# Optimization experiments

Hardware: AMD Instinct MI355X
Metric: run time of the kernel (lower is better)

Reference implementation:

```python
import jax, jax.numpy as jnp
import numpy as np

B, S, D = 1, 2048, 4096
H, KVH, HD = 32, 8, 128
ROPE_THETA = 10000.0


def setup_inputs() -> dict:
    key = jax.random.key(0)
    k1, k2, k3, k4, k5 = jax.random.split(key, 5)
    scale = D ** -0.5
    return {
        "hidden_states": jax.random.normal(k1, (B, S, D), dtype=jnp.float32),
        "position_ids": jnp.arange(S, dtype=jnp.int64).reshape(1, S),
        "Wq": jax.random.normal(k2, (H * HD, D), dtype=jnp.float32) * scale,
        "Wk": jax.random.normal(k3, (KVH * HD, D), dtype=jnp.float32) * scale,
        "Wv": jax.random.normal(k4, (KVH * HD, D), dtype=jnp.float32) * scale,
        "Wo": jax.random.normal(k5, (D, H * HD), dtype=jnp.float32) * scale,
    }


def _rotate_half(x):
    x1, x2 = x[..., : HD // 2], x[..., HD // 2 :]
    return jnp.concatenate((-x2, x1), axis=-1)


def reference(hidden_states, position_ids, Wq, Wk, Wv, Wo):
    b, s, d = hidden_states.shape
    # projections: nn.Linear applies x @ W.T
    q = jnp.einsum("bsd,ed->bse", hidden_states, Wq).reshape(b, s, H, HD).transpose(0, 2, 1, 3)
    k = jnp.einsum("bsd,ed->bse", hidden_states, Wk).reshape(b, s, KVH, HD).transpose(0, 2, 1, 3)
    v = jnp.einsum("bsd,ed->bse", hidden_states, Wv).reshape(b, s, KVH, HD).transpose(0, 2, 1, 3)
    # rotary embedding (default rope: inv_freq = theta^(-2i/d), attention_scaling = 1)
    inv_freq = 1.0 / (ROPE_THETA ** (jnp.arange(0, HD, 2, dtype=jnp.float32) / HD))
    pos = position_ids.astype(jnp.float32)  # [Bp, S]
    freqs = pos[:, :, None] * inv_freq[None, None, :]  # [Bp, S, HD/2]
    emb = jnp.concatenate((freqs, freqs), axis=-1)  # [Bp, S, HD]
    cos = jnp.cos(emb)[:, None, :, :]  # unsqueeze head dim
    sin = jnp.sin(emb)[:, None, :, :]
    q = q * cos + _rotate_half(q) * sin
    k = k * cos + _rotate_half(k) * sin
    # GQA: expand kv heads to match query heads
    groups = H // KVH
    k = jnp.repeat(k, groups, axis=1)
    v = jnp.repeat(v, groups, axis=1)
    # causal attention, scaling = head_dim^-0.5
    scores = jnp.einsum("bhqd,bhkd->bhqk", q, k) * (HD ** -0.5)
    causal = jnp.tril(jnp.ones((s, s), dtype=bool))
    scores = jnp.where(causal[None, None], scores, jnp.finfo(scores.dtype).min)
    attn = jax.nn.softmax(scores, axis=-1)
    out = jnp.einsum("bhqk,bhkd->bhqd", attn, v)
    out = out.transpose(0, 2, 1, 3).reshape(b, s, H * HD)
    return jnp.einsum("bse,de->bsd", out, Wo)
```

## Files before the change

### kernel.cpp

```cpp
#include <hip/hip_runtime.h>
#include <stdint.h>

typedef unsigned short u16;
typedef __attribute__((ext_vector_type(4))) float f32x4;
typedef __attribute__((ext_vector_type(8))) short bf16x8;

static constexpr int S   = 2048;
static constexpr int DM  = 4096;
static constexpr int NH  = 32;
static constexpr int NKV = 8;
static constexpr int HD  = 128;
static constexpr int LDQ = 5120;

__device__ __forceinline__ u16 f2bf(float f) {
    union { float f; unsigned u; } v; v.f = f;
    return (u16)((v.u + 0x7FFFu + ((v.u >> 16) & 1u)) >> 16);
}
__device__ __forceinline__ float bf2f(u16 h) {
    union { unsigned u; float f; } v; v.u = ((unsigned)h) << 16;
    return v.f;
}
__device__ __forceinline__ unsigned pk2bf(float lo, float hi) {
    unsigned r;
    asm("v_cvt_pk_bf16_f32 %0, %1, %2" : "=v"(r) : "v"(lo), "v"(hi));
    return r;
}

__device__ __forceinline__ void mfma16(f32x4& d, bf16x8 a, bf16x8 b) {
    asm("v_mfma_f32_16x16x32_bf16 %0, %1, %2, %0" : "+v"(d) : "v"(a), "v"(b));
}

__device__ __forceinline__ void gload_lds16(const u16* g, u16* lds) {
    __builtin_amdgcn_global_load_lds((__attribute__((address_space(1))) void*)g,
                                     (__attribute__((address_space(3))) void*)lds,
                                     16, 0, 0);
}

__global__ __launch_bounds__(256) void cvt_all(const float* __restrict__ X,
                                               const float* __restrict__ Wq,
                                               const float* __restrict__ Wk,
                                               const float* __restrict__ Wv,
                                               const float* __restrict__ Wo,
                                               u16* __restrict__ out) {
    const int n4 = 12582912;
    int i = blockIdx.x * blockDim.x + threadIdx.x;
    int stride = gridDim.x * blockDim.x;
    for (; i < n4; i += stride) {
        float4 v;
        if (i < 2097152)       v = ((const float4*)X)[i];
        else if (i < 6291456)  v = ((const float4*)Wq)[i - 2097152];
        else if (i < 7340032)  v = ((const float4*)Wk)[i - 6291456];
        else if (i < 8388608)  v = ((const float4*)Wv)[i - 7340032];
        else                   v = ((const float4*)Wo)[i - 8388608];
        ushort4 o;
        o.x = f2bf(v.x); o.y = f2bf(v.y); o.z = f2bf(v.z); o.w = f2bf(v.w);
        ((ushort4*)out)[i] = o;
    }
}

__global__ __launch_bounds__(256) void rope_table_kernel(float2* __restrict__ tbl) {
    int i = blockIdx.x * blockDim.x + threadIdx.x;
    if (i >= S * 64) return;
    int p = i >> 6, j = i & 63;
    float inv = powf(10000.0f, -(float)j / 64.0f);
    float a = (float)p * inv;
    tbl[i] = make_float2(cosf(a), sinf(a));
}

__global__ __launch_bounds__(256) void rope2_kernel(u16* __restrict__ X,
                                                    const float2* __restrict__ tbl,
                                                    float qscale) {
    int i = blockIdx.x * blockDim.x + threadIdx.x;
    const int total = S * 40 * 64;
    if (i >= total) return;
    int dd = i & 63;
    int t2 = i >> 6;
    int hh = t2 % 40;
    int s  = t2 / 40;
    size_t base;
    float scale;
    if (hh < 32) { base = (size_t)s * LDQ + hh * HD + dd;               scale = qscale; }
    else         { base = (size_t)s * LDQ + 4096 + (hh - 32) * HD + dd; scale = 1.0f;   }
    float x1 = bf2f(X[base]);
    float x2 = bf2f(X[base + 64]);
    float2 cs = tbl[(s << 6) + dd];
    X[base]      = f2bf((x1 * cs.x - x2 * cs.y) * scale);
    X[base + 64] = f2bf((x2 * cs.x + x1 * cs.y) * scale);
}

__global__ __launch_bounds__(256)
void gemm_bt(const u16* __restrict__ A, const u16* __restrict__ Bt,
             float* __restrict__ C, int M, int N, int K, int lda, int ldb, int ldc) {
    __shared__ u16 Al[128 * 64];
    __shared__ u16 Bl[128 * 64];
    const int t = threadIdx.x;
    const int w = t >> 6, l = t & 63;
    const int r16 = l & 15, g4 = l >> 4;
    const int m0 = blockIdx.y * 128, n0 = blockIdx.x * 128;
    const int wr = (w >> 1) * 64, wc = (w & 1) * 64;

    f32x4 acc[4][4];
#pragma unroll
    for (int i = 0; i < 4; ++i)
#pragma unroll
        for (int j = 0; j < 4; ++j) acc[i][j] = f32x4{0.f, 0.f, 0.f, 0.f};

    for (int kt = 0; kt < K; kt += 64) {
#pragma unroll
        for (int i = 0; i < 4; ++i) {
            int c = i * 256 + t;
            int r = c >> 3, s = (c & 7) ^ (r & 7);
            gload_lds16(A + (size_t)(m0 + r) * lda + kt + (s << 3),
                        Al + ((i * 256 + w * 64) << 3));
        }
#pragma unroll
        for (int i = 0; i < 4; ++i) {
            int c = i * 256 + t;
            int r = c >> 3, s = (c & 7) ^ (r & 7);
            gload_lds16(Bt + (size_t)(n0 + r) * ldb + kt + (s << 3),
                        Bl + ((i * 256 + w * 64) << 3));
        }
        asm volatile("s_waitcnt vmcnt(0)" ::: "memory");
        __syncthreads();

#pragma unroll
        for (int kk = 0; kk < 2; ++kk) {
            bf16x8 af[4], bfr[4];
#pragma unroll
            for (int mi = 0; mi < 4; ++mi) {
                int r = wr + mi * 16 + r16;
                af[mi] = *(const bf16x8*)((const char*)Al +
                          ((r * 128 + kk * 64 + g4 * 16) ^ ((r & 7) << 4)));
            }
#pragma unroll
            for (int ni = 0; ni < 4; ++ni) {
                int r = wc + ni * 16 + r16;
                bfr[ni] = *(const bf16x8*)((const char*)Bl +
                           ((r * 128 + kk * 64 + g4 * 16) ^ ((r & 7) << 4)));
            }
#pragma unroll
            for (int mi = 0; mi < 4; ++mi)
#pragma unroll
                for (int ni = 0; ni < 4; ++ni)
                    mfma16(acc[mi][ni], af[mi], bfr[ni]);
        }
        __syncthreads();
    }

    const int rb = g4 * 4;
#pragma unroll
    for (int mi = 0; mi < 4; ++mi)
#pragma unroll
        for (int ni = 0; ni < 4; ++ni) {
            const int n = n0 + wc + ni * 16 + r16;
            const int mbase = m0 + wr + mi * 16 + rb;
#pragma unroll
            for (int j = 0; j < 4; ++j)
                C[(size_t)(mbase + j) * ldc + n] = acc[mi][ni][j];
        }
}

__global__ __launch_bounds__(256)
void gemm_qkv(const u16* __restrict__ A, const u16* __restrict__ Bt,
              u16* __restrict__ Cqk, u16* __restrict__ Vt) {
    __shared__ u16 Al[128 * 64];
    __shared__ u16 Bl[128 * 64];
    const int t = threadIdx.x;
    const int w = t >> 6, l = t & 63;
    const int r16 = l & 15, g4 = l >> 4;
    const int m0 = blockIdx.y * 128, n0 = blockIdx.x * 128;
    const int wr = (w >> 1) * 64, wc = (w & 1) * 64;

    f32x4 acc[4][4];
#pragma unroll
    for (int i = 0; i < 4; ++i)
#pragma unroll
        for (int j = 0; j < 4; ++j) acc[i][j] = f32x4{0.f, 0.f, 0.f, 0.f};

    for (int kt = 0; kt < DM; kt += 64) {
#pragma unroll
        for (int i = 0; i < 4; ++i) {
            int c = i * 256 + t;
            int r = c >> 3, s = (c & 7) ^ (r & 7);
            gload_lds16(A + (size_t)(m0 + r) * DM + kt + (s << 3),
                        Al + ((i * 256 + w * 64) << 3));
        }
#pragma unroll
        for (int i = 0; i < 4; ++i) {
            int c = i * 256 + t;
            int r = c >> 3, s = (c & 7) ^ (r & 7);
            gload_lds16(Bt + (size_t)(n0 + r) * DM + kt + (s << 3),
                        Bl + ((i * 256 + w * 64) << 3));
        }
        asm volatile("s_waitcnt vmcnt(0)" ::: "memory");
        __syncthreads();

#pragma unroll
        for (int kk = 0; kk < 2; ++kk) {
            bf16x8 af[4], bfr[4];
#pragma unroll
            for (int mi = 0; mi < 4; ++mi) {
                int r = wr + mi * 16 + r16;
                af[mi] = *(const bf16x8*)((const char*)Al +
                          ((r * 128 + kk * 64 + g4 * 16) ^ ((r & 7) << 4)));
            }
#pragma unroll
            for (int ni = 0; ni < 4; ++ni) {
                int r = wc + ni * 16 + r16;
                bfr[ni] = *(const bf16x8*)((const char*)Bl +
                           ((r * 128 + kk * 64 + g4 * 16) ^ ((r & 7) << 4)));
            }
#pragma unroll
            for (int mi = 0; mi < 4; ++mi)
#pragma unroll
                for (int ni = 0; ni < 4; ++ni)
                    mfma16(acc[mi][ni], af[mi], bfr[ni]);
        }
        __syncthreads();
    }

    const int rb = g4 * 4;
    if (n0 < 5120) {
#pragma unroll
        for (int mi = 0; mi < 4; ++mi)
#pragma unroll
            for (int ni = 0; ni < 4; ++ni) {
                const int n = n0 + wc + ni * 16 + r16;
                const int mbase = m0 + wr + mi * 16 + rb;
#pragma unroll
                for (int j = 0; j < 4; ++j)
                    Cqk[(size_t)(mbase + j) * LDQ + n] = f2bf(acc[mi][ni][j]);
            }
    } else {
#pragma unroll
        for (int mi = 0; mi < 4; ++mi)
#pragma unroll
            for (int ni = 0; ni < 4; ++ni) {
                const int n = n0 + wc + ni * 16 + r16 - 5120;
                const int mbase = m0 + wr + mi * 16 + rb;
                ushort4 v4;
                v4.x = f2bf(acc[mi][ni][0]); v4.y = f2bf(acc[mi][ni][1]);
                v4.z = f2bf(acc[mi][ni][2]); v4.w = f2bf(acc[mi][ni][3]);
                *(ushort4*)&Vt[(size_t)n * S + mbase] = v4;
            }
    }
}

__global__ __launch_bounds__(256, 3)
void attn_fwd(const u16* __restrict__ QK, const u16* __restrict__ Vt,
              u16* __restrict__ O) {
    __shared__ u16 Kl[2][64 * 128];
    __shared__ u16 Vl[2][128 * 64];
    __shared__ u16 Pl[4 * 16 * 64];

    const int t = threadIdx.x;
    const int w = t >> 6, l = t & 63;
    const int r16 = l & 15, g4 = l >> 4;
    const int h = blockIdx.y;
    const int kvh = h >> 2;
    const int p = blockIdx.x;
    const int q0A = p * 64, q0B = (31 - p) * 64;
    const int ntA = p + 1, ntB = 32 - p;

    const u16* Kg = QK + 4096 + kvh * HD;
    const u16* Vg = Vt + (size_t)(kvh * HD) * S;
    u16* Pb = &Pl[w * 1024];

    bf16x8 qfA[4], qfB[4];
    {
        const u16* Qg = QK + h * HD;
        const size_t qrA = (size_t)(q0A + w * 16 + r16) * LDQ;
        const size_t qrB = (size_t)(q0B + w * 16 + r16) * LDQ;
#pragma unroll
        for (int kg = 0; kg < 4; ++kg) {
            qfA[kg] = *(const bf16x8*)&Qg[qrA + kg * 32 + g4 * 8];
            qfB[kg] = *(const bf16x8*)&Qg[qrB + kg * 32 + g4 * 8];
        }
    }

    f32x4 accA[8], accB[8];
    float mA[4], lA[4], mB[4], lB[4];
#pragma unroll
    for (int i = 0; i < 8; ++i) { accA[i] = f32x4{0,0,0,0}; accB[i] = f32x4{0,0,0,0}; }
#pragma unroll
    for (int j = 0; j < 4; ++j) { mA[j] = -3.0e38f; lA[j] = 0.f; mB[j] = -3.0e38f; lB[j] = 0.f; }

    auto stage = [&](int tk, int b) {
        const int kv0 = tk * 64;
#pragma unroll
        for (int i = 0; i < 4; ++i) {
            int c = i * 256 + t;
            int r = c >> 4, s = (c & 15) ^ (r & 7);
            gload_lds16(Kg + (size_t)(kv0 + r) * LDQ + (s << 3),
                        &Kl[b][0] + ((i * 256 + w * 64) << 3));
        }
#pragma unroll
        for (int i = 0; i < 4; ++i) {
            int c = i * 256 + t;
            int r = c >> 3, s = (c & 7) ^ (r & 7);
            gload_lds16(Vg + (size_t)r * S + kv0 + (s << 3),
                        &Vl[b][0] + ((i * 256 + w * 64) << 3));
        }
    };

    auto compute = [&](f32x4 (&acco)[8], float (&mrun)[4], float (&lrun)[4],
                       const bf16x8 (&qf)[4], int q0, int tk, bool maskit, int b) {
        const int kv0 = tk * 64;
        const u16* Kb = &Kl[b][0];
        const u16* Vb = &Vl[b][0];

        f32x4 sc[4];
#pragma unroll
        for (int ni = 0; ni < 4; ++ni) sc[ni] = f32x4{0,0,0,0};
        __builtin_amdgcn_s_setprio(1);
#pragma unroll
        for (int kg = 0; kg < 4; ++kg) {
#pragma unroll
            for (int ni = 0; ni < 4; ++ni) {
                int row = ni * 16 + r16;
                int bb = (row * 256 + kg * 64 + g4 * 16) ^ ((row & 7) << 4);
                bf16x8 kf = *(const bf16x8*)((const char*)Kb + bb);
                mfma16(sc[ni], qf[kg], kf);
            }
        }
        __builtin_amdgcn_s_setprio(0);

        float vmax[4];
        bool grow = false;
#pragma unroll
        for (int j = 0; j < 4; ++j) {
            if (maskit) {
                const int qg = q0 + w * 16 + g4 * 4 + j;
#pragma unroll
                for (int ni = 0; ni < 4; ++ni)
                    if (kv0 + ni * 16 + r16 > qg) sc[ni][j] = -3.0e38f;
            }
            float v = fmaxf(fmaxf(sc[0][j], sc[1][j]), fmaxf(sc[2][j], sc[3][j]));
            v = fmaxf(v, __shfl_xor(v, 1, 16));
            v = fmaxf(v, __shfl_xor(v, 2, 16));
            v = fmaxf(v, __shfl_xor(v, 4, 16));
            v = fmaxf(v, __shfl_xor(v, 8, 16));
            vmax[j] = v;
            grow = grow || (v > mrun[j] + 11.5f);
        }
        float fac[4] = {1.f, 1.f, 1.f, 1.f};
        if (__any(grow)) {
#pragma unroll
            for (int j = 0; j < 4; ++j) {
                float nm = fmaxf(mrun[j], vmax[j]);
                fac[j] = exp2f(mrun[j] - nm);
                mrun[j] = nm;
            }
#pragma unroll
            for (int i = 0; i < 8; ++i)
#pragma unroll
                for (int j = 0; j < 4; ++j) acco[i][j] *= fac[j];
        }
#pragma unroll
        for (int j = 0; j < 4; ++j) {
            float p0 = exp2f(sc[0][j] - mrun[j]);
            float p1 = exp2f(sc[1][j] - mrun[j]);
            float p2 = exp2f(sc[2][j] - mrun[j]);
            float p3 = exp2f(sc[3][j] - mrun[j]);
            sc[0][j] = p0; sc[1][j] = p1; sc[2][j] = p2; sc[3][j] = p3;
            float s2 = (p0 + p1) + (p2 + p3);
            s2 += __shfl_xor(s2, 1, 16);
            s2 += __shfl_xor(s2, 2, 16);
            s2 += __shfl_xor(s2, 4, 16);
            s2 += __shfl_xor(s2, 8, 16);
            lrun[j] = lrun[j] * fac[j] + s2;
        }

        {
            char* pp = (char*)Pb;
            const int rb_ = g4 * 4;
#pragma unroll
            for (int ni = 0; ni < 4; ++ni) {
                unsigned r01 = pk2bf(sc[ni][0], sc[ni][1]);
                unsigned r23 = pk2bf(sc[ni][2], sc[ni][3]);
                const int col2 = (ni * 16 + r16) << 1;
                *(u16*)(pp + (((rb_ + 0) * 128 + col2) ^ (((rb_ + 0) & 7) << 4))) = (u16)r01;
                *(u16*)(pp + (((rb_ + 1) * 128 + col2) ^ (((rb_ + 1) & 7) << 4))) = (u16)(r01 >> 16);
                *(u16*)(pp + (((rb_ + 2) * 128 + col2) ^ (((rb_ + 2) & 7) << 4))) = (u16)r23;
                *(u16*)(pp + (((rb_ + 3) * 128 + col2) ^ (((rb_ + 3) & 7) << 4))) = (u16)(r23 >> 16);
            }
        }
        asm volatile("s_waitcnt lgkmcnt(0)" ::: "memory");
        __builtin_amdgcn_sched_barrier(0);

        int pb0 = (r16 * 128 + g4 * 16) ^ ((r16 & 7) << 4);
        bf16x8 pf0 = *(const bf16x8*)((const char*)Pb + pb0);
        bf16x8 pf1 = *(const bf16x8*)((const char*)Pb + (pb0 ^ 64));
        __builtin_amdgcn_s_setprio(1);
#pragma unroll
        for (int ni = 0; ni < 8; ++ni) {
            int row = ni * 16 + r16;
            int bb = (row * 128 + g4 * 16) ^ ((row & 7) << 4);
            bf16x8 v0 = *(const bf16x8*)((const char*)Vb + bb);
            mfma16(acco[ni], pf0, v0);
            bf16x8 v1 = *(const bf16x8*)((const char*)Vb + (bb ^ 64));
            mfma16(acco[ni], pf1, v1);
        }
        __builtin_amdgcn_s_setprio(0);
    };

    auto epilogue = [&](f32x4 (&acco)[8], float (&lrun)[4], int q0) {
        float rl[4];
#pragma unroll
        for (int j = 0; j < 4; ++j) rl[j] = 1.0f / lrun[j];
#pragma unroll
        for (int ni = 0; ni < 8; ++ni)
#pragma unroll
            for (int j = 0; j < 4; ++j) {
                const int qg = q0 + w * 16 + g4 * 4 + j;
                O[(size_t)qg * DM + h * HD + ni * 16 + r16] = f2bf(acco[ni][j] * rl[j]);
            }
    };

    stage(0, 0);
    asm volatile("s_waitcnt vmcnt(0)" ::: "memory");
    __syncthreads();
    int buf = 0;

    for (int tk = 0; tk < ntB; ++tk) {
        if (tk + 1 < ntB) stage(tk + 1, buf ^ 1);
        compute(accB, mB, lB, qfB, q0B, tk, tk == ntB - 1, buf);
        if (tk < ntA) compute(accA, mA, lA, qfA, q0A, tk, tk == ntA - 1, buf);
        asm volatile("s_waitcnt vmcnt(0)" ::: "memory");
        __syncthreads();
        buf ^= 1;
    }
    epilogue(accA, lA, q0A);
    epilogue(accB, lB, q0B);
}

extern "C" void kernel_launch(void* const* d_in, const int* in_sizes, int n_in,
                              void* d_out, int out_size, void* d_ws, size_t ws_size,
                              hipStream_t stream) {
    const float* X  = (const float*)d_in[0];
    const float* Wq = (const float*)d_in[2];
    const float* Wk = (const float*)d_in[3];
    const float* Wv = (const float*)d_in[4];
    const float* Wo = (const float*)d_in[5];

    char* ws = (char*)d_ws;
    u16*    Xbf  = (u16*)(ws + 0);
    u16*    Wqkv = (u16*)(ws + 16777216);
    u16*    Wobf = (u16*)(ws + 67108864);
    u16*    QKb  = (u16*)(ws + 100663296);
    u16*    Vtbf = (u16*)(ws + 121634816);
    u16*    Obf  = (u16*)(ws + 125829120);
    float2* tbl  = (float2*)(ws + 142606336);
    if (ws_size < 143654912ull) return;

    dim3 blk(256);

    cvt_all<<<2048, blk, 0, stream>>>(X, Wq, Wk, Wv, Wo, (u16*)ws);
    rope_table_kernel<<<(S * 64 + 255) / 256, blk, 0, stream>>>(tbl);

    gemm_qkv<<<dim3(48, 16), blk, 0, stream>>>(Xbf, Wqkv, QKb, Vtbf);

    rope2_kernel<<<(S * 40 * 64 + 255) / 256, blk, 0, stream>>>(
        QKb, tbl, 0.08838834764831845f * 1.4426950408889634f);

    attn_fwd<<<dim3(16, NH), blk, 0, stream>>>(QKb, Vtbf, Obf);

    gemm_bt<<<dim3(DM / 128, S / 128), blk, 0, stream>>>(
        Obf, Wobf, (float*)d_out, S, DM, DM, DM, DM, DM);
}
```

Baseline: 362.5 us.

## Process two query heads sharing a KV head per attention block

The attention kernel now has each block handle one 64-row query tile for two adjacent heads that share a KV head. Previously each block paired two causal query tiles of a single head. Each K fragment loaded from LDS now feeds MFMAs for both heads, and each staged K/V tile is reused twice, cutting LDS reads and global K/V traffic per unit of work. Causal load balance now comes from interleaving short and long tiles through the block index rather than pairing them inside a block, so block runtimes vary more. Launch bounds drop to 2 waves-per-EU to make room for the doubled register state.

```diff
diff --git a/kernel.cpp b/kernel.cpp
--- a/kernel.cpp
+++ b/kernel.cpp
@@ -246,44 +246,45 @@
     }
 }
 
-__global__ __launch_bounds__(256, 3)
+__global__ __launch_bounds__(256, 2)
 void attn_fwd(const u16* __restrict__ QK, const u16* __restrict__ Vt,
               u16* __restrict__ O) {
     __shared__ u16 Kl[2][64 * 128];
     __shared__ u16 Vl[2][128 * 64];
-    __shared__ u16 Pl[4 * 16 * 64];
+    __shared__ u16 Pl[4 * 1024];
 
     const int t = threadIdx.x;
     const int w = t >> 6, l = t & 63;
     const int r16 = l & 15, g4 = l >> 4;
-    const int h = blockIdx.y;
-    const int kvh = h >> 2;
-    const int p = blockIdx.x;
-    const int q0A = p * 64, q0B = (31 - p) * 64;
-    const int ntA = p + 1, ntB = 32 - p;
+    const int xx = blockIdx.x;
+    const int tq = (xx & 1) ? (31 - (xx >> 1)) : (xx >> 1);
+    const int hp = blockIdx.y;
+    const int h0 = hp << 1;
+    const int kvh = hp >> 1;
+    const int q0 = tq * 64;
+    const int nt = tq + 1;
 
     const u16* Kg = QK + 4096 + kvh * HD;
     const u16* Vg = Vt + (size_t)(kvh * HD) * S;
     u16* Pb = &Pl[w * 1024];
 
-    bf16x8 qfA[4], qfB[4];
+    bf16x8 qf0[4], qf1[4];
     {
-        const u16* Qg = QK + h * HD;
-        const size_t qrA = (size_t)(q0A + w * 16 + r16) * LDQ;
-        const size_t qrB = (size_t)(q0B + w * 16 + r16) * LDQ;
+        const u16* Qg = QK + h0 * HD;
+        const size_t qr = (size_t)(q0 + w * 16 + r16) * LDQ;
 #pragma unroll
         for (int kg = 0; kg < 4; ++kg) {
-            qfA[kg] = *(const bf16x8*)&Qg[qrA + kg * 32 + g4 * 8];
-            qfB[kg] = *(const bf16x8*)&Qg[qrB + kg * 32 + g4 * 8];
-        }
-    }
-
-    f32x4 accA[8], accB[8];
-    float mA[4], lA[4], mB[4], lB[4];
-#pragma unroll
-    for (int i = 0; i < 8; ++i) { accA[i] = f32x4{0,0,0,0}; accB[i] = f32x4{0,0,0,0}; }
-#pragma unroll
-    for (int j = 0; j < 4; ++j) { mA[j] = -3.0e38f; lA[j] = 0.f; mB[j] = -3.0e38f; lB[j] = 0.f; }
+            qf0[kg] = *(const bf16x8*)&Qg[qr + kg * 32 + g4 * 8];
+            qf1[kg] = *(const bf16x8*)&Qg[qr + HD + kg * 32 + g4 * 8];
+        }
+    }
+
+    f32x4 acc0[8], acc1[8];
+    float mr0[4], lr0[4], mr1[4], lr1[4];
+#pragma unroll
+    for (int i = 0; i < 8; ++i) { acc0[i] = f32x4{0,0,0,0}; acc1[i] = f32x4{0,0,0,0}; }
+#pragma unroll
+    for (int j = 0; j < 4; ++j) { mr0[j] = -3.0e38f; lr0[j] = 0.f; mr1[j] = -3.0e38f; lr1[j] = 0.f; }
 
     auto stage = [&](int tk, int b) {
         const int kv0 = tk * 64;
@@ -303,28 +304,8 @@
         }
     };
 
-    auto compute = [&](f32x4 (&acco)[8], float (&mrun)[4], float (&lrun)[4],
-                       const bf16x8 (&qf)[4], int q0, int tk, bool maskit, int b) {
-        const int kv0 = tk * 64;
-        const u16* Kb = &Kl[b][0];
-        const u16* Vb = &Vl[b][0];
-
-        f32x4 sc[4];
-#pragma unroll
-        for (int ni = 0; ni < 4; ++ni) sc[ni] = f32x4{0,0,0,0};
-        __builtin_amdgcn_s_setprio(1);
-#pragma unroll
-        for (int kg = 0; kg < 4; ++kg) {
-#pragma unroll
-            for (int ni = 0; ni < 4; ++ni) {
-                int row = ni * 16 + r16;
-                int bb = (row * 256 + kg * 64 + g4 * 16) ^ ((row & 7) << 4);
-                bf16x8 kf = *(const bf16x8*)((const char*)Kb + bb);
-                mfma16(sc[ni], qf[kg], kf);
-            }
-        }
-        __builtin_amdgcn_s_setprio(0);
-
+    auto soft_pv = [&](f32x4 (&sc)[4], float (&mrun)[4], float (&lrun)[4],
+                       f32x4 (&acco)[8], const u16* Vb, int kv0, bool maskit) {
         float vmax[4];
         bool grow = false;
 #pragma unroll
@@ -404,34 +385,58 @@
         __builtin_amdgcn_s_setprio(0);
     };
 
-    auto epilogue = [&](f32x4 (&acco)[8], float (&lrun)[4], int q0) {
-        float rl[4];
-#pragma unroll
-        for (int j = 0; j < 4; ++j) rl[j] = 1.0f / lrun[j];
-#pragma unroll
-        for (int ni = 0; ni < 8; ++ni)
-#pragma unroll
-            for (int j = 0; j < 4; ++j) {
-                const int qg = q0 + w * 16 + g4 * 4 + j;
-                O[(size_t)qg * DM + h * HD + ni * 16 + r16] = f2bf(acco[ni][j] * rl[j]);
-            }
-    };
-
     stage(0, 0);
     asm volatile("s_waitcnt vmcnt(0)" ::: "memory");
     __syncthreads();
     int buf = 0;
 
-    for (int tk = 0; tk < ntB; ++tk) {
-        if (tk + 1 < ntB) stage(tk + 1, buf ^ 1);
-        compute(accB, mB, lB, qfB, q0B, tk, tk == ntB - 1, buf);
-        if (tk < ntA) compute(accA, mA, lA, qfA, q0A, tk, tk == ntA - 1, buf);
+    for (int tk = 0; tk < nt; ++tk) {
+        if (tk + 1 < nt) stage(tk + 1, buf ^ 1);
+        const int kv0 = tk * 64;
+        const bool maskit = (tk == nt - 1);
+        const u16* Kb = &Kl[buf][0];
+        const u16* Vb = &Vl[buf][0];
+
+        f32x4 sc0[4], sc1[4];
+#pragma unroll
+        for (int ni = 0; ni < 4; ++ni) { sc0[ni] = f32x4{0,0,0,0}; sc1[ni] = f32x4{0,0,0,0}; }
+        __builtin_amdgcn_s_setprio(1);
+#pragma unroll
+        for (int kg = 0; kg < 4; ++kg) {
+#pragma unroll
+            for (int ni = 0; ni < 4; ++ni) {
+                int row = ni * 16 + r16;
+                int bb = (row * 256 + kg * 64 + g4 * 16) ^ ((row & 7) << 4);
+                bf16x8 kf = *(const bf16x8*)((const char*)Kb + bb);
+                mfma16(sc0[ni], qf0[kg], kf);
+                mfma16(sc1[ni], qf1[kg], kf);
+            }
+        }
+        __builtin_amdgcn_s_setprio(0);
+
+        soft_pv(sc0, mr0, lr0, acc0, Vb, kv0, maskit);
+        __builtin_amdgcn_sched_barrier(0);
+        soft_pv(sc1, mr1, lr1, acc1, Vb, kv0, maskit);
+
         asm volatile("s_waitcnt vmcnt(0)" ::: "memory");
         __syncthreads();
         buf ^= 1;
     }
-    epilogue(accA, lA, q0A);
-    epilogue(accB, lB, q0B);
+
+    {
+        float rl0[4], rl1[4];
+#pragma unroll
+        for (int j = 0; j < 4; ++j) { rl0[j] = 1.0f / lr0[j]; rl1[j] = 1.0f / lr1[j]; }
+#pragma unroll
+        for (int ni = 0; ni < 8; ++ni)
+#pragma unroll
+            for (int j = 0; j < 4; ++j) {
+                const int qg = q0 + w * 16 + g4 * 4 + j;
+                const int dd = ni * 16 + r16;
+                O[(size_t)qg * DM + h0 * HD + dd]      = f2bf(acc0[ni][j] * rl0[j]);
+                O[(size_t)qg * DM + h0 * HD + HD + dd] = f2bf(acc1[ni][j] * rl1[j]);
+            }
+    }
 }
 
 extern "C" void kernel_launch(void* const* d_in, const int* in_sizes, int n_in,
@@ -463,7 +468,7 @@
     rope2_kernel<<<(S * 40 * 64 + 255) / 256, blk, 0, stream>>>(
         QKb, tbl, 0.08838834764831845f * 1.4426950408889634f);
 
-    attn_fwd<<<dim3(16, NH), blk, 0, stream>>>(QKb, Vtbf, Obf);
+    attn_fwd<<<dim3(32, 16), blk, 0, stream>>>(QKb, Vtbf, Obf);
 
     gemm_bt<<<dim3(DM / 128, S / 128), blk, 0, stream>>>(
         Obf, Wobf, (float*)d_out, S, DM, DM, DM, DM, DM);
```

Result: slower. 416.0 us (+14.8%).

## Transpose QK^T MFMA so each lane owns one query row for softmax

Applied to the files above, without the earlier changes.

Swaps the MFMA operand order for the score computation so each lane holds 16 scores of a single query row instead of 4 rows. The row max and sum then reduce mostly in registers, with two cross-lane shuffles instead of four per row, and each row keeps a single running max and sum. P is written to LDS as packed 32-bit stores rather than 16-bit scatter stores. Rescale factors and reciprocals are broadcast back to the accumulator layout with shuffles. The launch bounds occupancy hint also drops from 3 to 2, which gives the compiler more registers at the cost of fewer resident waves.

```diff
diff --git a/kernel.cpp b/kernel.cpp
--- a/kernel.cpp
+++ b/kernel.cpp
@@ -246,12 +246,12 @@
     }
 }
 
-__global__ __launch_bounds__(256, 3)
+__global__ __launch_bounds__(256, 2)
 void attn_fwd(const u16* __restrict__ QK, const u16* __restrict__ Vt,
               u16* __restrict__ O) {
     __shared__ u16 Kl[2][64 * 128];
     __shared__ u16 Vl[2][128 * 64];
-    __shared__ u16 Pl[4 * 16 * 64];
+    __shared__ u16 Pl[4 * 1024];
 
     const int t = threadIdx.x;
     const int w = t >> 6, l = t & 63;
@@ -279,11 +279,9 @@
     }
 
     f32x4 accA[8], accB[8];
-    float mA[4], lA[4], mB[4], lB[4];
+    float mA = -3.0e38f, lA = 0.f, mB = -3.0e38f, lB = 0.f;
 #pragma unroll
     for (int i = 0; i < 8; ++i) { accA[i] = f32x4{0,0,0,0}; accB[i] = f32x4{0,0,0,0}; }
-#pragma unroll
-    for (int j = 0; j < 4; ++j) { mA[j] = -3.0e38f; lA[j] = 0.f; mB[j] = -3.0e38f; lB[j] = 0.f; }
 
     auto stage = [&](int tk, int b) {
         const int kv0 = tk * 64;
@@ -303,7 +301,7 @@
         }
     };
 
-    auto compute = [&](f32x4 (&acco)[8], float (&mrun)[4], float (&lrun)[4],
+    auto compute = [&](f32x4 (&acco)[8], float& mrun, float& lrun,
                        const bf16x8 (&qf)[4], int q0, int tk, bool maskit, int b) {
         const int kv0 = tk * 64;
         const u16* Kb = &Kl[b][0];
@@ -320,69 +318,64 @@
                 int row = ni * 16 + r16;
                 int bb = (row * 256 + kg * 64 + g4 * 16) ^ ((row & 7) << 4);
                 bf16x8 kf = *(const bf16x8*)((const char*)Kb + bb);
-                mfma16(sc[ni], qf[kg], kf);
+                mfma16(sc[ni], kf, qf[kg]);
             }
         }
         __builtin_amdgcn_s_setprio(0);
 
-        float vmax[4];
-        bool grow = false;
-#pragma unroll
-        for (int j = 0; j < 4; ++j) {
-            if (maskit) {
-                const int qg = q0 + w * 16 + g4 * 4 + j;
-#pragma unroll
-                for (int ni = 0; ni < 4; ++ni)
-                    if (kv0 + ni * 16 + r16 > qg) sc[ni][j] = -3.0e38f;
-            }
-            float v = fmaxf(fmaxf(sc[0][j], sc[1][j]), fmaxf(sc[2][j], sc[3][j]));
-            v = fmaxf(v, __shfl_xor(v, 1, 16));
-            v = fmaxf(v, __shfl_xor(v, 2, 16));
-            v = fmaxf(v, __shfl_xor(v, 4, 16));
-            v = fmaxf(v, __shfl_xor(v, 8, 16));
-            vmax[j] = v;
-            grow = grow || (v > mrun[j] + 11.5f);
-        }
-        float fac[4] = {1.f, 1.f, 1.f, 1.f};
-        if (__any(grow)) {
-#pragma unroll
-            for (int j = 0; j < 4; ++j) {
-                float nm = fmaxf(mrun[j], vmax[j]);
-                fac[j] = exp2f(mrun[j] - nm);
-                mrun[j] = nm;
-            }
+        const int qg = q0 + (w << 4) + r16;
+        if (maskit) {
+#pragma unroll
+            for (int ni = 0; ni < 4; ++ni)
+#pragma unroll
+                for (int j = 0; j < 4; ++j)
+                    if (kv0 + ni * 16 + g4 * 4 + j > qg) sc[ni][j] = -3.0e38f;
+        }
+
+        float v = fmaxf(fmaxf(fmaxf(sc[0][0], sc[0][1]), fmaxf(sc[0][2], sc[0][3])),
+                        fmaxf(fmaxf(sc[1][0], sc[1][1]), fmaxf(sc[1][2], sc[1][3])));
+        v = fmaxf(v, fmaxf(fmaxf(fmaxf(sc[2][0], sc[2][1]), fmaxf(sc[2][2], sc[2][3])),
+                           fmaxf(fmaxf(sc[3][0], sc[3][1]), fmaxf(sc[3][2], sc[3][3]))));
+        v = fmaxf(v, __shfl_xor(v, 16));
+        v = fmaxf(v, __shfl_xor(v, 32));
+
+        float facl = 1.f;
+        if (__any(v > mrun + 11.5f)) {
+            float nm = fmaxf(mrun, v);
+            facl = exp2f(mrun - nm);
+            mrun = nm;
+            float fj[4];
+#pragma unroll
+            for (int j = 0; j < 4; ++j) fj[j] = __shfl(facl, g4 * 4 + j, 16);
 #pragma unroll
             for (int i = 0; i < 8; ++i)
 #pragma unroll
-                for (int j = 0; j < 4; ++j) acco[i][j] *= fac[j];
-        }
-#pragma unroll
-        for (int j = 0; j < 4; ++j) {
-            float p0 = exp2f(sc[0][j] - mrun[j]);
-            float p1 = exp2f(sc[1][j] - mrun[j]);
-            float p2 = exp2f(sc[2][j] - mrun[j]);
-            float p3 = exp2f(sc[3][j] - mrun[j]);
-            sc[0][j] = p0; sc[1][j] = p1; sc[2][j] = p2; sc[3][j] = p3;
-            float s2 = (p0 + p1) + (p2 + p3);
-            s2 += __shfl_xor(s2, 1, 16);
-            s2 += __shfl_xor(s2, 2, 16);
-            s2 += __shfl_xor(s2, 4, 16);
-            s2 += __shfl_xor(s2, 8, 16);
-            lrun[j] = lrun[j] * fac[j] + s2;
-        }
+                for (int j = 0; j < 4; ++j) acco[i][j] *= fj[j];
+        }
+#pragma unroll
+        for (int ni = 0; ni < 4; ++ni)
+#pragma unroll
+            for (int j = 0; j < 4; ++j) sc[ni][j] = exp2f(sc[ni][j] - mrun);
+
+        float s2 = ((sc[0][0] + sc[0][1]) + (sc[0][2] + sc[0][3]))
+                 + ((sc[1][0] + sc[1][1]) + (sc[1][2] + sc[1][3]))
+                 + ((sc[2][0] + sc[2][1]) + (sc[2][2] + sc[2][3]))
+                 + ((sc[3][0] + sc[3][1]) + (sc[3][2] + sc[3][3]));
+        s2 += __shfl_xor(s2, 16);
+        s2 += __shfl_xor(s2, 32);
+        lrun = lrun * facl + s2;
 
         {
             char* pp = (char*)Pb;
-            const int rb_ = g4 * 4;
-#pragma unroll
-            for (int ni = 0; ni < 4; ++ni) {
-                unsigned r01 = pk2bf(sc[ni][0], sc[ni][1]);
-                unsigned r23 = pk2bf(sc[ni][2], sc[ni][3]);
-                const int col2 = (ni * 16 + r16) << 1;
-                *(u16*)(pp + (((rb_ + 0) * 128 + col2) ^ (((rb_ + 0) & 7) << 4))) = (u16)r01;
-                *(u16*)(pp + (((rb_ + 1) * 128 + col2) ^ (((rb_ + 1) & 7) << 4))) = (u16)(r01 >> 16);
-                *(u16*)(pp + (((rb_ + 2) * 128 + col2) ^ (((rb_ + 2) & 7) << 4))) = (u16)r23;
-                *(u16*)(pp + (((rb_ + 3) * 128 + col2) ^ (((rb_ + 3) & 7) << 4))) = (u16)(r23 >> 16);
+            const int swz = (r16 & 7) << 4;
+            const int rowb = r16 * 128;
+#pragma unroll
+            for (int ti = 0; ti < 4; ++ti) {
+                unsigned r01 = pk2bf(sc[ti][0], sc[ti][1]);
+                unsigned r23 = pk2bf(sc[ti][2], sc[ti][3]);
+                const int colb = (ti * 16 + g4 * 4) << 1;
+                *(unsigned*)(pp + ((rowb + colb) ^ swz))     = r01;
+                *(unsigned*)(pp + ((rowb + colb + 4) ^ swz)) = r23;
             }
         }
         asm volatile("s_waitcnt lgkmcnt(0)" ::: "memory");
@@ -404,10 +397,11 @@
         __builtin_amdgcn_s_setprio(0);
     };
 
-    auto epilogue = [&](f32x4 (&acco)[8], float (&lrun)[4], int q0) {
+    auto epilogue = [&](f32x4 (&acco)[8], float lrun, int q0) {
+        float rlr = 1.0f / lrun;
         float rl[4];
 #pragma unroll
-        for (int j = 0; j < 4; ++j) rl[j] = 1.0f / lrun[j];
+        for (int j = 0; j < 4; ++j) rl[j] = __shfl(rlr, g4 * 4 + j, 16);
 #pragma unroll
         for (int ni = 0; ni < 8; ++ni)
 #pragma unroll
```

After: 339.2 us, median of 2. 1.07x faster.
